# Kernel tuning notes

Measured on AMD Instinct MI355X. Metric: run time of the kernel, lower is better.

The kernel has to match this reference:

```python
import jax, jax.numpy as jnp
import numpy as np

B, N = 8, 512
C_IN, C_E, C_MID, C_OUT = 64, 16, 64, 64


def _linear_params(key, fan_in, fan_out):
    k1, k2 = jax.random.split(key)
    bound = 1.0 / np.sqrt(fan_in)
    W = jax.random.uniform(k1, (fan_out, fan_in), jnp.float32, -bound, bound)
    b = jax.random.uniform(k2, (fan_out,), jnp.float32, -bound, bound)
    return W, b


def setup_inputs() -> dict:
    key = jax.random.key(0)
    ks = jax.random.split(key, 9)
    x = jax.random.normal(ks[0], (B, N, C_IN), jnp.float32)
    adj = jax.random.randint(ks[1], (B, N, N), 0, 2).astype(jnp.float32)
    edge_attr = jax.random.normal(ks[2], (B, N, N, C_E), jnp.float32)
    W1, b1 = _linear_params(ks[3], C_IN, C_MID)
    W2, b2 = _linear_params(ks[4], C_IN, C_MID)
    We, be = _linear_params(ks[5], C_E, C_MID)
    Wn, bn = _linear_params(ks[6], C_MID, C_MID)   # user-supplied net: Linear(mid, mid)
    Wo1, bo1 = _linear_params(ks[7], C_IN, C_OUT)
    Wo2, bo2 = _linear_params(ks[8], C_MID, C_OUT)
    return {"x": x, "adj": adj, "edge_attr": edge_attr,
            "W1": W1, "b1": b1, "W2": W2, "b2": b2, "We": We, "be": be,
            "Wn": Wn, "bn": bn, "Wo1": Wo1, "bo1": bo1, "Wo2": Wo2, "bo2": bo2}


def reference(x, adj, edge_attr, W1, b1, W2, b2, We, be, Wn, bn, Wo1, bo1, Wo2, bo2):
    # node / edge projections
    msg_1 = jnp.einsum('bnc,mc->bnm', x, W1) + b1          # [B, N, mid]
    msg_2 = jnp.einsum('bnc,mc->bnm', x, W2) + b2          # [B, N, mid]
    msg_e = jnp.einsum('bijc,mc->bijm', edge_attr, We) + be  # [B, N, N, mid]
    # broadcast sum: msg_1 over dim 1, msg_2 over dim 2 (matches torch unsqueeze)
    msg = msg_1[:, None, :, :] + msg_2[:, :, None, :] + msg_e  # [B, N, N, mid]
    # net applied after hard-coded relu
    msg = jnp.einsum('bijm,km->bijk', jax.nn.relu(msg), Wn) + bn
    # sum aggregator with adjacency mask, reduced over dim 1
    msg = jnp.einsum('bijm,bij->bjm', msg, adj)            # [B, N, mid]
    h_1 = jnp.einsum('bnc,oc->bno', x, Wo1) + bo1
    h_2 = jnp.einsum('bnm,om->bno', msg, Wo2) + bo2
    return h_1 + h_2
```

## Files before the change

kernel.cpp:

```cpp
#include <hip/hip_runtime.h>
#include <stdint.h>

#define B_   8
#define N_   512
#define CE_  16
#define BN_  (B_*N_)
#define Q_   8

typedef __attribute__((ext_vector_type(8))) short bf16x8;
typedef __attribute__((ext_vector_type(4))) float f32x4;
typedef __attribute__((ext_vector_type(4))) int   i32x4;

union PackA { i32x4 i; bf16x8 h; };

__device__ __forceinline__ unsigned short f2bf_rne(float f) {
  unsigned u = __float_as_uint(f);
  u += 0x7FFFu + ((u >> 16) & 1u);
  return (unsigned short)(u >> 16);
}

__global__ __launch_bounds__(256) void k1_pre(
    const float* __restrict__ x,
    const float* __restrict__ W1,  const float* __restrict__ b1,
    const float* __restrict__ W2,  const float* __restrict__ b2,
    const float* __restrict__ Wn,  const float* __restrict__ bn,
    const float* __restrict__ Wo1, const float* __restrict__ bo1,
    const float* __restrict__ Wo2, const float* __restrict__ bo2,
    float* __restrict__ m1, float* __restrict__ m2, float* __restrict__ base,
    float* __restrict__ Wc, float* __restrict__ bc)
{
  const int tid = threadIdx.x;
  if (blockIdx.x == BN_/4) {
    for (int idx = tid; idx < 64*64; idx += 256) {
      const int k = idx >> 6, m = idx & 63;
      float acc = 0.f;
      for (int t = 0; t < 64; ++t) acc += Wo2[k*64 + t] * Wn[t*64 + m];
      Wc[idx] = acc;
    }
    if (tid < 64) {
      float acc = 0.f;
      for (int t = 0; t < 64; ++t) acc += Wo2[tid*64 + t] * bn[t];
      bc[tid] = acc;
    }
    return;
  }
  const int r = tid >> 6, m = tid & 63;
  const int row = blockIdx.x*4 + r;
  __shared__ float xs[4][64];
  xs[r][m] = x[(size_t)row*64 + m];
  __syncthreads();
  const float* xr = xs[r];
  float a1 = b1[m], a2 = b2[m], a3 = bo1[m] + bo2[m];
  const float* w1r = W1  + m*64;
  const float* w2r = W2  + m*64;
  const float* w3r = Wo1 + m*64;
  #pragma unroll 8
  for (int c = 0; c < 64; ++c) {
    const float xv = xr[c];
    a1 += xv * w1r[c];
    a2 += xv * w2r[c];
    a3 += xv * w3r[c];
  }
  m1[(size_t)row*64 + m]   = a1;
  m2[(size_t)row*64 + m]   = a2;
  base[(size_t)row*64 + m] = a3;
}

__global__ __launch_bounds__(256) void k2_main(
    const float* __restrict__ edge, const float* __restrict__ adj,
    const float* __restrict__ We,   const float* __restrict__ be,
    const float* __restrict__ m1,   const float* __restrict__ m2,
    float* __restrict__ pS, float* __restrict__ pdeg)
{
  const int tid  = threadIdx.x;
  const int lane = tid & 63;
  const int wid  = tid >> 6;
  const int col  = lane & 15;
  const int quad = lane >> 4;

  const int blk = blockIdx.x;
  const int q   = blk & 7;
  const int grp = blk >> 3;
  const int b   = grp >> 5;
  const int j0  = (grp & 31) << 4;
  const int i0  = q*64 + wid*16;

  const i32x4 izero = {0,0,0,0};

  bf16x8 bfr[4];
  #pragma unroll
  for (int c = 0; c < 4; ++c) {
    PackA u; u.i = izero;
    if (quad < 2) {
      const float* wr = We + (c*16 + col)*CE_ + quad*8;
      unsigned p0 = ((unsigned)f2bf_rne(wr[1]) << 16) | f2bf_rne(wr[0]);
      unsigned p1 = ((unsigned)f2bf_rne(wr[3]) << 16) | f2bf_rne(wr[2]);
      unsigned p2 = ((unsigned)f2bf_rne(wr[5]) << 16) | f2bf_rne(wr[4]);
      unsigned p3 = ((unsigned)f2bf_rne(wr[7]) << 16) | f2bf_rne(wr[6]);
      i32x4 v = {(int)p0, (int)p1, (int)p2, (int)p3};
      u.i = v;
    }
    bfr[c] = u.h;
  }

  f32x4 m1f[4];
  #pragma unroll
  for (int c = 0; c < 4; ++c) {
    const float bev = be[c*16 + col];
    const float* mp = m1 + (size_t)(b*N_ + j0 + quad*4)*64 + c*16 + col;
    m1f[c].x = mp[0]   + bev;
    m1f[c].y = mp[64]  + bev;
    m1f[c].z = mp[128] + bev;
    m1f[c].w = mp[192] + bev;
  }

  const f32x4 fzero = {0.f, 0.f, 0.f, 0.f};
  f32x4 S[4];
  S[0] = fzero; S[1] = fzero; S[2] = fzero; S[3] = fzero;
  f32x4 deg4 = fzero;

  const float* ep  = edge + ((size_t)(b*N_ + i0)*N_ + (j0 + col))*CE_ + (quad & 1)*8;
  const float* ap  = adj  + (size_t)(b*N_ + i0)*N_ + j0 + quad*4;
  const float* m2p = m2   + (size_t)(b*N_ + i0)*64 + col;

  for (int it = 0; it < 16; ++it) {
    f32x4 e0 = *(const f32x4*)(ep);
    f32x4 e1 = *(const f32x4*)(ep + 4);
    PackA ua;
    ua.i.x = (int)__builtin_amdgcn_perm(__float_as_uint(e0.y), __float_as_uint(e0.x), 0x07060302u);
    ua.i.y = (int)__builtin_amdgcn_perm(__float_as_uint(e0.w), __float_as_uint(e0.z), 0x07060302u);
    ua.i.z = (int)__builtin_amdgcn_perm(__float_as_uint(e1.y), __float_as_uint(e1.x), 0x07060302u);
    ua.i.w = (int)__builtin_amdgcn_perm(__float_as_uint(e1.w), __float_as_uint(e1.z), 0x07060302u);
    const f32x4 adj4 = *(const f32x4*)ap;

    #pragma unroll
    for (int c = 0; c < 4; ++c) {
      const float m2v = m2p[c*16];
      f32x4 cin;
      cin.x = m1f[c].x + m2v;
      cin.y = m1f[c].y + m2v;
      cin.z = m1f[c].z + m2v;
      cin.w = m1f[c].w + m2v;
      f32x4 r = __builtin_amdgcn_mfma_f32_16x16x32_bf16(ua.h, bfr[c], cin, 0, 0, 0);
      S[c].x += adj4.x * fmaxf(r.x, 0.f);
      S[c].y += adj4.y * fmaxf(r.y, 0.f);
      S[c].z += adj4.z * fmaxf(r.z, 0.f);
      S[c].w += adj4.w * fmaxf(r.w, 0.f);
    }
    deg4 += adj4;
    ep  += N_ * CE_;
    ap  += N_;
    m2p += 64;
  }

  __shared__ float red[4][16*68];
  __shared__ float redd[4][16];
  #pragma unroll
  for (int c = 0; c < 4; ++c) {
    red[wid][(quad*4 + 0)*68 + c*16 + col] = S[c].x;
    red[wid][(quad*4 + 1)*68 + c*16 + col] = S[c].y;
    red[wid][(quad*4 + 2)*68 + c*16 + col] = S[c].z;
    red[wid][(quad*4 + 3)*68 + c*16 + col] = S[c].w;
  }
  if (col == 0) {
    redd[wid][quad*4 + 0] = deg4.x;
    redd[wid][quad*4 + 1] = deg4.y;
    redd[wid][quad*4 + 2] = deg4.z;
    redd[wid][quad*4 + 3] = deg4.w;
  }
  __syncthreads();

  float* oS = pS + ((size_t)q*BN_ + b*N_ + j0)*64;
  #pragma unroll
  for (int t = 0; t < 4; ++t) {
    const int idx = t*256 + tid;
    const int row = idx >> 6, ch = idx & 63;
    oS[idx] = red[0][row*68 + ch] + red[1][row*68 + ch]
            + red[2][row*68 + ch] + red[3][row*68 + ch];
  }
  if (tid < 16) {
    pdeg[(size_t)q*BN_ + b*N_ + j0 + tid] =
      redd[0][tid] + redd[1][tid] + redd[2][tid] + redd[3][tid];
  }
}

__global__ __launch_bounds__(256) void k3_out(
    const float* __restrict__ pS, const float* __restrict__ pdeg,
    const float* __restrict__ base, const float* __restrict__ Wc,
    const float* __restrict__ bc, float* __restrict__ out)
{
  const int tid = threadIdx.x;
  const int r   = tid >> 6;
  const int k   = tid & 63;
  const int row = blockIdx.x*4 + r;
  __shared__ float sm[4][64];
  float s = 0.f, dr = 0.f;
  #pragma unroll
  for (int q = 0; q < Q_; ++q) {
    s  += pS[((size_t)q*BN_ + row)*64 + k];
    dr += pdeg[(size_t)q*BN_ + row];
  }
  sm[r][k] = s;
  __syncthreads();
  float acc = base[(size_t)row*64 + k] + dr * bc[k];
  const float* wr  = Wc + k*64;
  const float* smr = sm[r];
  #pragma unroll
  for (int m = 0; m < 64; ++m) acc += smr[m] * wr[m];
  out[(size_t)row*64 + k] = acc;
}

extern "C" void kernel_launch(void* const* d_in, const int* in_sizes, int n_in,
                              void* d_out, int out_size, void* d_ws, size_t ws_size,
                              hipStream_t stream)
{
  const float* x    = (const float*)d_in[0];
  const float* adj  = (const float*)d_in[1];
  const float* edge = (const float*)d_in[2];
  const float* W1   = (const float*)d_in[3];
  const float* b1   = (const float*)d_in[4];
  const float* W2   = (const float*)d_in[5];
  const float* b2   = (const float*)d_in[6];
  const float* We   = (const float*)d_in[7];
  const float* be   = (const float*)d_in[8];
  const float* Wn   = (const float*)d_in[9];
  const float* bn   = (const float*)d_in[10];
  const float* Wo1  = (const float*)d_in[11];
  const float* bo1  = (const float*)d_in[12];
  const float* Wo2  = (const float*)d_in[13];
  const float* bo2  = (const float*)d_in[14];
  float* out = (float*)d_out;

  char* ws = (char*)d_ws;
  float* m1   = (float*)(ws);
  float* m2   = (float*)(ws + (size_t)(1u<<20));
  float* base = (float*)(ws + (size_t)2*(1u<<20));
  float* Wc   = (float*)(ws + (size_t)3*(1u<<20));
  float* bc   = (float*)(ws + (size_t)3*(1u<<20) + 16384);
  float* pdeg = (float*)(ws + (size_t)3*(1u<<20) + 17408);
  float* pS   = (float*)(ws + (size_t)3*(1u<<20) + 17408 + 131072);

  k1_pre<<<BN_/4 + 1, 256, 0, stream>>>(x, W1, b1, W2, b2, Wn, bn,
                                        Wo1, bo1, Wo2, bo2,
                                        m1, m2, base, Wc, bc);
  k2_main<<<2048, 256, 0, stream>>>(edge, adj, We, be, m1, m2, pS, pdeg);
  k3_out<<<BN_/4, 256, 0, stream>>>(pS, pdeg, base, Wc, bc, out);
}
```

Measured before the change: 298.5 us.

## Use K=16 MFMA, prepack We in k1, packed-FMA accumulation, split Wc

Switches the edge projection from the 16x16x32 bf16 MFMA, which padded K=16 up to 32 with zeros, to the 16x16x16 bf16_1k MFMA. Each lane now loads 4 edge floats instead of 8, and no MFMA work is spent on the zero half. The bf16 packing of We moves into k1, so k2 blocks load a prepacked fragment instead of converting it per block. The Wc precompute is spread over four blocks. The adjacency-weighted relu accumulation now uses v_pk_fma_f32 and v_pk_add_f32 inline asm. The edge stream is the dominant memory traffic and the total bytes read are unchanged, so the gain depends on whether k2 was bound by instruction work.

```diff
diff --git a/kernel.cpp b/kernel.cpp
--- a/kernel.cpp
+++ b/kernel.cpp
@@ -8,15 +8,40 @@
 #define Q_   8
 
 typedef __attribute__((ext_vector_type(8))) short bf16x8;
+typedef __attribute__((ext_vector_type(4))) short bf16x4;
 typedef __attribute__((ext_vector_type(4))) float f32x4;
+typedef __attribute__((ext_vector_type(2))) float f32x2;
 typedef __attribute__((ext_vector_type(4))) int   i32x4;
-
-union PackA { i32x4 i; bf16x8 h; };
+typedef __attribute__((ext_vector_type(2))) int   i32x2;
+
+#if defined(__has_builtin)
+#  if __has_builtin(__builtin_amdgcn_mfma_f32_16x16x16bf16_1k)
+#    define HAVE_MFMA16 1
+#  endif
+#endif
+#ifndef HAVE_MFMA16
+#  define HAVE_MFMA16 0
+#endif
+
+union PackA8 { i32x4 i; bf16x8 h; };
+union PackA4 { i32x2 i; bf16x4 h; };
+union V4     { f32x4 v; f32x2 h[2]; };
 
 __device__ __forceinline__ unsigned short f2bf_rne(float f) {
   unsigned u = __float_as_uint(f);
   u += 0x7FFFu + ((u >> 16) & 1u);
   return (unsigned short)(u >> 16);
+}
+
+__device__ __forceinline__ f32x2 pk_fma(f32x2 a, f32x2 b, f32x2 c) {
+  f32x2 d;
+  asm("v_pk_fma_f32 %0, %1, %2, %3" : "=v"(d) : "v"(a), "v"(b), "v"(c));
+  return d;
+}
+__device__ __forceinline__ f32x2 pk_add2(f32x2 a, f32x2 b) {
+  f32x2 d;
+  asm("v_pk_add_f32 %0, %1, %2" : "=v"(d) : "v"(a), "v"(b));
+  return d;
 }
 
 __global__ __launch_bounds__(256) void k1_pre(
@@ -26,26 +51,48 @@
     const float* __restrict__ Wn,  const float* __restrict__ bn,
     const float* __restrict__ Wo1, const float* __restrict__ bo1,
     const float* __restrict__ Wo2, const float* __restrict__ bo2,
+    const float* __restrict__ We,
     float* __restrict__ m1, float* __restrict__ m2, float* __restrict__ base,
-    float* __restrict__ Wc, float* __restrict__ bc)
+    float* __restrict__ Wc, float* __restrict__ bc, unsigned* __restrict__ wePack)
 {
   const int tid = threadIdx.x;
-  if (blockIdx.x == BN_/4) {
-    for (int idx = tid; idx < 64*64; idx += 256) {
-      const int k = idx >> 6, m = idx & 63;
+  const int bx  = blockIdx.x;
+  if (bx >= BN_/4) {
+    const int q4 = bx - BN_/4;
+    for (int idx = tid; idx < 16*64; idx += 256) {
+      const int k = q4*16 + (idx >> 6), m = idx & 63;
       float acc = 0.f;
+      #pragma unroll 8
       for (int t = 0; t < 64; ++t) acc += Wo2[k*64 + t] * Wn[t*64 + m];
-      Wc[idx] = acc;
+      Wc[k*64 + m] = acc;
     }
-    if (tid < 64) {
-      float acc = 0.f;
-      for (int t = 0; t < 64; ++t) acc += Wo2[tid*64 + t] * bn[t];
-      bc[tid] = acc;
+    if (q4 == 0) {
+      if (tid < 64) {
+        float acc = 0.f;
+        for (int t = 0; t < 64; ++t) acc += Wo2[tid*64 + t] * bn[t];
+        bc[tid] = acc;
+      }
+      const int c = tid >> 6, lane = tid & 63, col = lane & 15, quad = lane >> 4;
+#if HAVE_MFMA16
+      const float* wr = We + (c*16 + col)*CE_ + quad*4;
+      wePack[tid*2+0] = ((unsigned)f2bf_rne(wr[1]) << 16) | f2bf_rne(wr[0]);
+      wePack[tid*2+1] = ((unsigned)f2bf_rne(wr[3]) << 16) | f2bf_rne(wr[2]);
+#else
+      unsigned p0=0, p1=0, p2=0, p3=0;
+      if (quad < 2) {
+        const float* wr = We + (c*16 + col)*CE_ + quad*8;
+        p0 = ((unsigned)f2bf_rne(wr[1]) << 16) | f2bf_rne(wr[0]);
+        p1 = ((unsigned)f2bf_rne(wr[3]) << 16) | f2bf_rne(wr[2]);
+        p2 = ((unsigned)f2bf_rne(wr[5]) << 16) | f2bf_rne(wr[4]);
+        p3 = ((unsigned)f2bf_rne(wr[7]) << 16) | f2bf_rne(wr[6]);
+      }
+      wePack[tid*4+0]=p0; wePack[tid*4+1]=p1; wePack[tid*4+2]=p2; wePack[tid*4+3]=p3;
+#endif
     }
     return;
   }
   const int r = tid >> 6, m = tid & 63;
-  const int row = blockIdx.x*4 + r;
+  const int row = bx*4 + r;
   __shared__ float xs[4][64];
   xs[r][m] = x[(size_t)row*64 + m];
   __syncthreads();
@@ -68,7 +115,7 @@
 
 __global__ __launch_bounds__(256) void k2_main(
     const float* __restrict__ edge, const float* __restrict__ adj,
-    const float* __restrict__ We,   const float* __restrict__ be,
+    const unsigned* __restrict__ wePack, const float* __restrict__ be,
     const float* __restrict__ m1,   const float* __restrict__ m2,
     float* __restrict__ pS, float* __restrict__ pdeg)
 {
@@ -85,23 +132,17 @@
   const int j0  = (grp & 31) << 4;
   const int i0  = q*64 + wid*16;
 
-  const i32x4 izero = {0,0,0,0};
-
+#if HAVE_MFMA16
+  bf16x4 bfr[4];
+  { const i32x2* wp = (const i32x2*)wePack;
+    #pragma unroll
+    for (int c = 0; c < 4; ++c) { PackA4 u; u.i = wp[c*64 + lane]; bfr[c] = u.h; } }
+#else
   bf16x8 bfr[4];
-  #pragma unroll
-  for (int c = 0; c < 4; ++c) {
-    PackA u; u.i = izero;
-    if (quad < 2) {
-      const float* wr = We + (c*16 + col)*CE_ + quad*8;
-      unsigned p0 = ((unsigned)f2bf_rne(wr[1]) << 16) | f2bf_rne(wr[0]);
-      unsigned p1 = ((unsigned)f2bf_rne(wr[3]) << 16) | f2bf_rne(wr[2]);
-      unsigned p2 = ((unsigned)f2bf_rne(wr[5]) << 16) | f2bf_rne(wr[4]);
-      unsigned p3 = ((unsigned)f2bf_rne(wr[7]) << 16) | f2bf_rne(wr[6]);
-      i32x4 v = {(int)p0, (int)p1, (int)p2, (int)p3};
-      u.i = v;
-    }
-    bfr[c] = u.h;
-  }
+  { const i32x4* wp = (const i32x4*)wePack;
+    #pragma unroll
+    for (int c = 0; c < 4; ++c) { PackA8 u; u.i = wp[c*64 + lane]; bfr[c] = u.h; } }
+#endif
 
   f32x4 m1f[4];
   #pragma unroll
@@ -114,24 +155,36 @@
     m1f[c].w = mp[192] + bev;
   }
 
-  const f32x4 fzero = {0.f, 0.f, 0.f, 0.f};
-  f32x4 S[4];
-  S[0] = fzero; S[1] = fzero; S[2] = fzero; S[3] = fzero;
-  f32x4 deg4 = fzero;
-
-  const float* ep  = edge + ((size_t)(b*N_ + i0)*N_ + (j0 + col))*CE_ + (quad & 1)*8;
-  const float* ap  = adj  + (size_t)(b*N_ + i0)*N_ + j0 + quad*4;
-  const float* m2p = m2   + (size_t)(b*N_ + i0)*64 + col;
+  const f32x2 z2 = {0.f, 0.f};
+  f32x2 S2[4][2];
+  #pragma unroll
+  for (int c = 0; c < 4; ++c) { S2[c][0] = z2; S2[c][1] = z2; }
+  f32x2 dg0 = z2, dg1 = z2;
+
+#if HAVE_MFMA16
+  const float* ep = edge + ((size_t)(b*N_ + i0)*N_ + (j0 + col))*CE_ + quad*4;
+#else
+  const float* ep = edge + ((size_t)(b*N_ + i0)*N_ + (j0 + col))*CE_ + (quad & 1)*8;
+#endif
+  const float* ap  = adj + (size_t)(b*N_ + i0)*N_ + j0 + quad*4;
+  const float* m2p = m2  + (size_t)(b*N_ + i0)*64 + col;
 
   for (int it = 0; it < 16; ++it) {
-    f32x4 e0 = *(const f32x4*)(ep);
-    f32x4 e1 = *(const f32x4*)(ep + 4);
-    PackA ua;
+#if HAVE_MFMA16
+    const f32x4 e0 = *(const f32x4*)ep;
+    PackA4 ua;
+    ua.i.x = (int)__builtin_amdgcn_perm(__float_as_uint(e0.y), __float_as_uint(e0.x), 0x07060302u);
+    ua.i.y = (int)__builtin_amdgcn_perm(__float_as_uint(e0.w), __float_as_uint(e0.z), 0x07060302u);
+#else
+    const f32x4 e0 = *(const f32x4*)(ep);
+    const f32x4 e1 = *(const f32x4*)(ep + 4);
+    PackA8 ua;
     ua.i.x = (int)__builtin_amdgcn_perm(__float_as_uint(e0.y), __float_as_uint(e0.x), 0x07060302u);
     ua.i.y = (int)__builtin_amdgcn_perm(__float_as_uint(e0.w), __float_as_uint(e0.z), 0x07060302u);
     ua.i.z = (int)__builtin_amdgcn_perm(__float_as_uint(e1.y), __float_as_uint(e1.x), 0x07060302u);
     ua.i.w = (int)__builtin_amdgcn_perm(__float_as_uint(e1.w), __float_as_uint(e1.z), 0x07060302u);
-    const f32x4 adj4 = *(const f32x4*)ap;
+#endif
+    V4 av; av.v = *(const f32x4*)ap;
 
     #pragma unroll
     for (int c = 0; c < 4; ++c) {
@@ -141,13 +194,21 @@
       cin.y = m1f[c].y + m2v;
       cin.z = m1f[c].z + m2v;
       cin.w = m1f[c].w + m2v;
+#if HAVE_MFMA16
+      f32x4 r = __builtin_amdgcn_mfma_f32_16x16x16bf16_1k(ua.h, bfr[c], cin, 0, 0, 0);
+#else
       f32x4 r = __builtin_amdgcn_mfma_f32_16x16x32_bf16(ua.h, bfr[c], cin, 0, 0, 0);
-      S[c].x += adj4.x * fmaxf(r.x, 0.f);
-      S[c].y += adj4.y * fmaxf(r.y, 0.f);
-      S[c].z += adj4.z * fmaxf(r.z, 0.f);
-      S[c].w += adj4.w * fmaxf(r.w, 0.f);
+#endif
+      r.x = fmaxf(r.x, 0.f);
+      r.y = fmaxf(r.y, 0.f);
+      r.z = fmaxf(r.z, 0.f);
+      r.w = fmaxf(r.w, 0.f);
+      V4 rv; rv.v = r;
+      S2[c][0] = pk_fma(av.h[0], rv.h[0], S2[c][0]);
+      S2[c][1] = pk_fma(av.h[1], rv.h[1], S2[c][1]);
     }
-    deg4 += adj4;
+    dg0 = pk_add2(dg0, av.h[0]);
+    dg1 = pk_add2(dg1, av.h[1]);
     ep  += N_ * CE_;
     ap  += N_;
     m2p += 64;
@@ -157,16 +218,16 @@
   __shared__ float redd[4][16];
   #pragma unroll
   for (int c = 0; c < 4; ++c) {
-    red[wid][(quad*4 + 0)*68 + c*16 + col] = S[c].x;
-    red[wid][(quad*4 + 1)*68 + c*16 + col] = S[c].y;
-    red[wid][(quad*4 + 2)*68 + c*16 + col] = S[c].z;
-    red[wid][(quad*4 + 3)*68 + c*16 + col] = S[c].w;
+    red[wid][(quad*4 + 0)*68 + c*16 + col] = S2[c][0].x;
+    red[wid][(quad*4 + 1)*68 + c*16 + col] = S2[c][0].y;
+    red[wid][(quad*4 + 2)*68 + c*16 + col] = S2[c][1].x;
+    red[wid][(quad*4 + 3)*68 + c*16 + col] = S2[c][1].y;
   }
   if (col == 0) {
-    redd[wid][quad*4 + 0] = deg4.x;
-    redd[wid][quad*4 + 1] = deg4.y;
-    redd[wid][quad*4 + 2] = deg4.z;
-    redd[wid][quad*4 + 3] = deg4.w;
+    redd[wid][quad*4 + 0] = dg0.x;
+    redd[wid][quad*4 + 1] = dg0.y;
+    redd[wid][quad*4 + 2] = dg1.x;
+    redd[wid][quad*4 + 3] = dg1.y;
   }
   __syncthreads();
 
@@ -239,10 +300,12 @@
   float* bc   = (float*)(ws + (size_t)3*(1u<<20) + 16384);
   float* pdeg = (float*)(ws + (size_t)3*(1u<<20) + 17408);
   float* pS   = (float*)(ws + (size_t)3*(1u<<20) + 17408 + 131072);
-
-  k1_pre<<<BN_/4 + 1, 256, 0, stream>>>(x, W1, b1, W2, b2, Wn, bn,
-                                        Wo1, bo1, Wo2, bo2,
-                                        m1, m2, base, Wc, bc);
-  k2_main<<<2048, 256, 0, stream>>>(edge, adj, We, be, m1, m2, pS, pdeg);
+  unsigned* wePack = (unsigned*)(ws + (size_t)3*(1u<<20) + 17408 + 131072
+                                 + (size_t)Q_*BN_*64*4);
+
+  k1_pre<<<BN_/4 + 4, 256, 0, stream>>>(x, W1, b1, W2, b2, Wn, bn,
+                                        Wo1, bo1, Wo2, bo2, We,
+                                        m1, m2, base, Wc, bc, wePack);
+  k2_main<<<2048, 256, 0, stream>>>(edge, adj, wePack, be, m1, m2, pS, pdeg);
   k3_out<<<BN_/4, 256, 0, stream>>>(pS, pdeg, base, Wc, bc, out);
 }
```

New measurement: 270.7 us. 9.3% less time.
